# Optimization experiments

Measured on AMD Instinct MI355X. Metric: run time of the kernel, lower is better.

Reference implementation:

```python
import jax, jax.numpy as jnp
import numpy as np

IN_FEATURES = 4096
OUT_FEATURES = 4096
GROUPS = 1
QB = 2 ** (8 - 1) - 1  # 127, int8 absmax quant


def setup_inputs() -> dict:
    key = jax.random.key(0)
    k_x, k_w = jax.random.split(key)
    x = jax.random.normal(k_x, (8192, IN_FEATURES), dtype=jnp.float32)
    # kaiming_uniform_(a=sqrt(5)) -> uniform(-1/sqrt(in), 1/sqrt(in))
    bound = 1.0 / np.sqrt(IN_FEATURES)
    weight = jax.random.uniform(
        k_w, (OUT_FEATURES, IN_FEATURES), dtype=jnp.float32,
        minval=-bound, maxval=bound)
    return {"input": x, "weight": weight}


def reference(input, weight):
    # --- ternarize weight per group ---
    w = weight.reshape(GROUPS, -1)                       # [G, out*in/G]
    w = w - jnp.mean(w, axis=1, keepdims=True)
    w = jnp.sign(w)
    # beta: per-group scale (note denominator uses full element count, as in source)
    beta = jnp.sum(jnp.abs(w), axis=1, keepdims=True) / (w.shape[0] * w.shape[1])
    w = (w * beta).reshape(OUT_FEATURES, IN_FEATURES)    # [out, in]

    # --- absmax int8 quantize activations (quantized values used, not dequant) ---
    scale = QB / jnp.max(jnp.abs(input))
    quant = jnp.round(scale * input)                     # [tokens, in]

    # --- linear + rescale ---
    out = quant @ w.T                                    # [tokens, out]
    out = out / beta.reshape(-1, 1)                      # groups=1: scalar divide
    return out
```

## Files before the change

### kernel.cpp

```cpp
#include <hip/hip_runtime.h>
#include <hip/hip_bf16.h>

typedef __attribute__((ext_vector_type(4))) int int4v;

#define TOKENS 8192
#define IN_F   4096
#define OUT_F  4096


__global__ __launch_bounds__(256) void k_pre(const float4* __restrict__ w,
                                             const float4* __restrict__ x,
                                             double* __restrict__ partials,
                                             float* __restrict__ xpart) {
  if (blockIdx.x < 1024) {
    __shared__ double sm[256];
    double s = 0.0;
    const float4* p = w + (size_t)blockIdx.x * 4096;
    for (int i = threadIdx.x; i < 4096; i += 256) {
      float4 v = p[i];
      s += (double)v.x + (double)v.y + (double)v.z + (double)v.w;
    }
    sm[threadIdx.x] = s;
    __syncthreads();
    for (int off = 128; off > 0; off >>= 1) {
      if (threadIdx.x < off) sm[threadIdx.x] += sm[threadIdx.x + off];
      __syncthreads();
    }
    if (threadIdx.x == 0) partials[blockIdx.x] = sm[0];
  } else {
    const int b = blockIdx.x - 1024;
    float m = 0.f;
    const size_t n = (size_t)TOKENS * IN_F / 4;
    for (size_t i = (size_t)b * 256 + threadIdx.x; i < n; i += (size_t)1024 * 256) {
      float4 v = x[i];
      m = fmaxf(m, fmaxf(fmaxf(fabsf(v.x), fabsf(v.y)),
                         fmaxf(fabsf(v.z), fabsf(v.w))));
    }
    __shared__ float smf[256];
    smf[threadIdx.x] = m;
    __syncthreads();
    for (int off = 128; off > 0; off >>= 1) {
      if (threadIdx.x < off) smf[threadIdx.x] = fmaxf(smf[threadIdx.x], smf[threadIdx.x + off]);
      __syncthreads();
    }
    if (threadIdx.x == 0) xpart[b] = smf[0];
  }
}

__global__ __launch_bounds__(256) void k_finalize(double* __restrict__ hdr,
                                                  const double* __restrict__ partials,
                                                  const float* __restrict__ xpart) {
  __shared__ double sm[256];
  __shared__ float smf[256];
  double s = partials[threadIdx.x] + partials[threadIdx.x + 256] +
             partials[threadIdx.x + 512] + partials[threadIdx.x + 768];
  float m = fmaxf(fmaxf(xpart[threadIdx.x], xpart[threadIdx.x + 256]),
                  fmaxf(xpart[threadIdx.x + 512], xpart[threadIdx.x + 768]));
  sm[threadIdx.x] = s;
  smf[threadIdx.x] = m;
  __syncthreads();
  for (int off = 128; off > 0; off >>= 1) {
    if (threadIdx.x < off) {
      sm[threadIdx.x] += sm[threadIdx.x + off];
      smf[threadIdx.x] = fmaxf(smf[threadIdx.x], smf[threadIdx.x + off]);
    }
    __syncthreads();
  }
  if (threadIdx.x == 0) {
    hdr[0] = sm[0] / (double)((size_t)OUT_F * IN_F);
    hdr[1] = 127.0 / (double)smf[0];
  }
}

#define QB_BLK ((TOKENS * IN_F / 4) / 256)
#define TB_BLK ((OUT_F * IN_F / 4) / 256)
__global__ __launch_bounds__(256) void k_quant_tern(const float4* __restrict__ x,
                                                    const float4* __restrict__ w,
                                                    int* __restrict__ q,
                                                    int* __restrict__ sgn,
                                                    const double* __restrict__ hdr) {
  if (blockIdx.x < QB_BLK) {
    const double s = hdr[1];
    size_t i = (size_t)blockIdx.x * 256 + threadIdx.x;
    float4 v = x[i];
    int a = (int)rint(s * (double)v.x);
    int b = (int)rint(s * (double)v.y);
    int c = (int)rint(s * (double)v.z);
    int d = (int)rint(s * (double)v.w);
    q[i] = (a & 255) | ((b & 255) << 8) | ((c & 255) << 16) | ((d & 255) << 24);
  } else {
    const double m = hdr[0];
    size_t i = (size_t)(blockIdx.x - QB_BLK) * 256 + threadIdx.x;
    float4 v = w[i];
    int a = ((double)v.x > m) - ((double)v.x < m);
    int b = ((double)v.y > m) - ((double)v.y < m);
    int c = ((double)v.z > m) - ((double)v.z < m);
    int d = ((double)v.w > m) - ((double)v.w < m);
    sgn[i] = (a & 255) | ((b & 255) << 8) | ((c & 255) << 16) | ((d & 255) << 24);
  }
}

__global__ __launch_bounds__(512, 2) void k_gemm(const signed char* __restrict__ q,
                                                 const signed char* __restrict__ s,
                                                 float* __restrict__ out) {
  __shared__ signed char sA[4][256 * 64];
  __shared__ signed char sB[4][256 * 64];
  const int tid  = threadIdx.x;
  const int lane = tid & 63;
  const int wid  = tid >> 6;
  const int wm   = wid >> 2;
  const int wn   = wid & 3;
  const int l15  = lane & 15, l4 = lane >> 4;

  const int swz = (blockIdx.x & 7) * 64 + (blockIdx.x >> 3);
  const int bm = swz >> 4;
  const int bn = swz & 15;
  const size_t row0 = (size_t)bm * 256;
  const size_t col0 = (size_t)bn * 256;

  const int lane_off = l15 * 64 + ((l4 ^ ((l15 >> 1) & 3)) << 4);

#define SB0() __builtin_amdgcn_sched_barrier(0)

#define STAGE_AB(KT, BUF)                                                       \
  do {                                                                          \
    const int kt_ = (KT);                                                       \
    _Pragma("unroll")                                                           \
    for (int u = 0; u < 2; ++u) {                                               \
      const int slot = u * 512 + tid;                                           \
      const int r = slot >> 2, sir = slot & 3;                                  \
      const int koff = ((sir ^ ((r >> 1) & 3)) << 4);                           \
      const int ldst = (u * 512 + wid * 64) * 16;                               \
      __builtin_amdgcn_global_load_lds(                                         \
          (const __attribute__((address_space(1))) void*)(q + (row0 + (size_t)r) * IN_F + kt_ * 64 + koff), \
          (__attribute__((address_space(3))) void*)(sA[BUF] + ldst), 16, 0, 0); \
    }                                                                           \
    _Pragma("unroll")                                                           \
    for (int u = 0; u < 2; ++u) {                                               \
      const int slot = u * 512 + tid;                                           \
      const int r = slot >> 2, sir = slot & 3;                                  \
      const int koff = ((sir ^ ((r >> 1) & 3)) << 4);                           \
      const int ldst = (u * 512 + wid * 64) * 16;                               \
      __builtin_amdgcn_global_load_lds(                                         \
          (const __attribute__((address_space(1))) void*)(s + (col0 + (size_t)r) * IN_F + kt_ * 64 + koff), \
          (__attribute__((address_space(3))) void*)(sB[BUF] + ldst), 16, 0, 0); \
    }                                                                           \
  } while (0)

#define READ12(BUF, AV, BV)                                                     \
  do {                                                                          \
    _Pragma("unroll")                                                           \
    for (int f = 0; f < 8; ++f)                                                 \
      AV[f] = *(const int4v*)(sA[BUF] + (wm * 128 + f * 16) * 64 + lane_off);   \
    _Pragma("unroll")                                                           \
    for (int f = 0; f < 4; ++f)                                                 \
      BV[f] = *(const int4v*)(sB[BUF] + (wn * 64 + f * 16) * 64 + lane_off);    \
  } while (0)

#define MFMA32(AV, BV)                                                          \
  do {                                                                          \
    _Pragma("unroll")                                                           \
    for (int m_ = 0; m_ < 8; ++m_)                                              \
      _Pragma("unroll")                                                         \
      for (int n_ = 0; n_ < 4; ++n_)                                            \
        acc[m_][n_] = __builtin_amdgcn_mfma_i32_16x16x64_i8(AV[m_], BV[n_],     \
                                                            acc[m_][n_], 0, 0, 0); \
  } while (0)

#define BODY(KT, RBUF, SBUF, ACUR, BCUR, ANXT, BNXT)                            \
  do {                                                                          \
    asm volatile("s_waitcnt vmcnt(4)" ::: "memory");                            \
    SB0();                                                                      \
    __builtin_amdgcn_s_barrier();                                               \
    SB0();                                                                      \
    READ12(RBUF, ANXT, BNXT);                                                   \
    STAGE_AB(((KT) + 3) & 63, SBUF);                                            \
    SB0();                                                                      \
    asm volatile("s_waitcnt lgkmcnt(12)" ::: "memory");                         \
    SB0();                                                                      \
    __builtin_amdgcn_s_setprio(1);                                              \
    MFMA32(ACUR, BCUR);                                                         \
    __builtin_amdgcn_s_setprio(0);                                              \
    SB0();                                                                      \
  } while (0)

  int4v acc[8][4];
#pragma unroll
  for (int i = 0; i < 8; ++i)
#pragma unroll
    for (int j = 0; j < 4; ++j) acc[i][j] = int4v{0, 0, 0, 0};

  int4v aX[8], bX[4], aY[8], bY[4];

  STAGE_AB(0, 0);
  STAGE_AB(1, 1);
  STAGE_AB(2, 2);
  SB0();
  asm volatile("s_waitcnt vmcnt(8)" ::: "memory");
  SB0();
  __builtin_amdgcn_s_barrier();
  SB0();
  READ12(0, aX, bX);
  SB0();

  for (int kt = 0; kt < 64; kt += 4) {
    BODY(kt + 0, 1, 3, aX, bX, aY, bY);
    BODY(kt + 1, 2, 0, aY, bY, aX, bX);
    BODY(kt + 2, 3, 1, aX, bX, aY, bY);
    BODY(kt + 3, 0, 2, aY, bY, aX, bX);
  }

#pragma unroll
  for (int m = 0; m < 8; ++m)
#pragma unroll
    for (int n = 0; n < 4; ++n)
#pragma unroll
      for (int r = 0; r < 4; ++r) {
        const size_t rg = row0 + wm * 128 + m * 16 + l4 * 4 + r;
        const size_t cg = col0 + wn * 64 + n * 16 + l15;
        out[rg * OUT_F + cg] = (float)acc[m][n][r];
      }

#undef SB0
#undef STAGE_AB
#undef READ12
#undef MFMA32
#undef BODY
}

extern "C" void kernel_launch(void* const* d_in, const int* in_sizes, int n_in,
                              void* d_out, int out_size, void* d_ws, size_t ws_size,
                              hipStream_t stream) {
  const float* x = (const float*)d_in[0];
  const float* w = (const float*)d_in[1];
  float* out = (float*)d_out;

  char* ws = (char*)d_ws;
  double*   hdr      = (double*)ws;
  double*   partials = (double*)(ws + 1024);
  float*    xpart    = (float*)(ws + 9216);
  signed char* qbuf  = (signed char*)(ws + 16384);
  signed char* sbuf  = (signed char*)(ws + 16384 + (size_t)TOKENS * IN_F);

  k_pre<<<2048, 256, 0, stream>>>((const float4*)w, (const float4*)x, partials, xpart);
  k_finalize<<<1, 256, 0, stream>>>(hdr, partials, xpart);
  k_quant_tern<<<QB_BLK + TB_BLK, 256, 0, stream>>>((const float4*)x, (const float4*)w,
                                                    (int*)qbuf, (int*)sbuf, hdr);
  k_gemm<<<(TOKENS / 256) * (OUT_F / 256), 512, 0, stream>>>(qbuf, sbuf, out);
}
```

Baseline: 227.1 us.

## Restructure int8 GEMM mainloop to double-buffered K=128 tiles with ping-pong phases

Replaces the 4-stage K=64 LDS ring with a 2-stage ring of K=128 tiles and splits each tile's work into four barrier-separated MFMA phases. Global-to-LDS staging for A and B is interleaved between the phases. The LDS swizzle changes to an 8-way XOR over 128-byte rows. The aim is to halve the number of main-loop iterations and overlap loads with compute in a ping-pong style. In exchange it adds several extra barriers per tile, uses full vmcnt(0) waits, and keeps less prefetch depth in flight.

```diff
diff --git a/kernel.cpp b/kernel.cpp
--- a/kernel.cpp
+++ b/kernel.cpp
@@ -103,8 +103,8 @@
 __global__ __launch_bounds__(512, 2) void k_gemm(const signed char* __restrict__ q,
                                                  const signed char* __restrict__ s,
                                                  float* __restrict__ out) {
-  __shared__ signed char sA[4][256 * 64];
-  __shared__ signed char sB[4][256 * 64];
+  __shared__ signed char sA[2][256 * 128];
+  __shared__ signed char sB[2][256 * 128];
   const int tid  = threadIdx.x;
   const int lane = tid & 63;
   const int wid  = tid >> 6;
@@ -118,70 +118,99 @@
   const size_t row0 = (size_t)bm * 256;
   const size_t col0 = (size_t)bn * 256;
 
-  const int lane_off = l15 * 64 + ((l4 ^ ((l15 >> 1) & 3)) << 4);
+  const int xr = l15 & 7;
+  const int ksl0 = ((l4 ^ xr) << 4);
+  const int ksl1 = (((4 + l4) ^ xr) << 4);
+  const int aRowBase = (wm * 128 + l15) * 128;
+  const int bRowBase = (wn * 64 + l15) * 128;
 
 #define SB0() __builtin_amdgcn_sched_barrier(0)
 
-#define STAGE_AB(KT, BUF)                                                       \
+#define STAGE_T(GSRC, GROW0, KT, LDSBASE)                                       \
   do {                                                                          \
     const int kt_ = (KT);                                                       \
     _Pragma("unroll")                                                           \
-    for (int u = 0; u < 2; ++u) {                                               \
-      const int slot = u * 512 + tid;                                           \
-      const int r = slot >> 2, sir = slot & 3;                                  \
-      const int koff = ((sir ^ ((r >> 1) & 3)) << 4);                           \
-      const int ldst = (u * 512 + wid * 64) * 16;                               \
+    for (int u = 0; u < 4; ++u) {                                               \
+      const int d = u * 512 + tid;                                              \
+      const int r = d >> 3, p = d & 7;                                          \
+      const int koff = ((p ^ (r & 7)) << 4);                                    \
       __builtin_amdgcn_global_load_lds(                                         \
-          (const __attribute__((address_space(1))) void*)(q + (row0 + (size_t)r) * IN_F + kt_ * 64 + koff), \
-          (__attribute__((address_space(3))) void*)(sA[BUF] + ldst), 16, 0, 0); \
+          (const __attribute__((address_space(1))) void*)((GSRC) + ((GROW0) + (size_t)r) * IN_F + kt_ * 128 + koff), \
+          (__attribute__((address_space(3))) void*)((LDSBASE) + (u * 512 + wid * 64) * 16), 16, 0, 0); \
     }                                                                           \
-    _Pragma("unroll")                                                           \
-    for (int u = 0; u < 2; ++u) {                                               \
-      const int slot = u * 512 + tid;                                           \
-      const int r = slot >> 2, sir = slot & 3;                                  \
-      const int koff = ((sir ^ ((r >> 1) & 3)) << 4);                           \
-      const int ldst = (u * 512 + wid * 64) * 16;                               \
-      __builtin_amdgcn_global_load_lds(                                         \
-          (const __attribute__((address_space(1))) void*)(s + (col0 + (size_t)r) * IN_F + kt_ * 64 + koff), \
-          (__attribute__((address_space(3))) void*)(sB[BUF] + ldst), 16, 0, 0); \
-    }                                                                           \
-  } while (0)
-
-#define READ12(BUF, AV, BV)                                                     \
+  } while (0)
+
+#define RD_A8(BUF, AV, KSL)                                                     \
   do {                                                                          \
     _Pragma("unroll")                                                           \
     for (int f = 0; f < 8; ++f)                                                 \
-      AV[f] = *(const int4v*)(sA[BUF] + (wm * 128 + f * 16) * 64 + lane_off);   \
+      AV[f] = *(const int4v*)(sA[BUF] + aRowBase + f * 2048 + (KSL));           \
+  } while (0)
+
+#define RD_B2(BUF, BV, NB0, KSL)                                                \
+  do {                                                                          \
+    BV[0] = *(const int4v*)(sB[BUF] + bRowBase + (NB0) * 2048 + (KSL));         \
+    BV[1] = *(const int4v*)(sB[BUF] + bRowBase + ((NB0) + 1) * 2048 + (KSL));   \
+  } while (0)
+
+#define MFMA16(AV, BV, NB)                                                      \
+  do {                                                                          \
     _Pragma("unroll")                                                           \
-    for (int f = 0; f < 4; ++f)                                                 \
-      BV[f] = *(const int4v*)(sB[BUF] + (wn * 64 + f * 16) * 64 + lane_off);    \
-  } while (0)
-
-#define MFMA32(AV, BV)                                                          \
-  do {                                                                          \
-    _Pragma("unroll")                                                           \
-    for (int m_ = 0; m_ < 8; ++m_)                                              \
-      _Pragma("unroll")                                                         \
-      for (int n_ = 0; n_ < 4; ++n_)                                            \
-        acc[m_][n_] = __builtin_amdgcn_mfma_i32_16x16x64_i8(AV[m_], BV[n_],     \
-                                                            acc[m_][n_], 0, 0, 0); \
-  } while (0)
-
-#define BODY(KT, RBUF, SBUF, ACUR, BCUR, ANXT, BNXT)                            \
-  do {                                                                          \
-    asm volatile("s_waitcnt vmcnt(4)" ::: "memory");                            \
+    for (int m_ = 0; m_ < 8; ++m_) {                                            \
+      acc[m_][NB]     = __builtin_amdgcn_mfma_i32_16x16x64_i8(AV[m_], BV[0],    \
+                                                              acc[m_][NB], 0, 0, 0); \
+      acc[m_][NB + 1] = __builtin_amdgcn_mfma_i32_16x16x64_i8(AV[m_], BV[1],    \
+                                                              acc[m_][NB + 1], 0, 0, 0); \
+    }                                                                           \
+  } while (0)
+
+#define PH_ENTER()                                                              \
+  SB0();                                                                        \
+  __builtin_amdgcn_s_barrier();                                                 \
+  asm volatile("s_waitcnt lgkmcnt(0)" ::: "memory");                            \
+  SB0();                                                                        \
+  __builtin_amdgcn_s_setprio(1)
+
+#define PH_EXIT()                                                               \
+  __builtin_amdgcn_s_setprio(0);                                                \
+  SB0();                                                                        \
+  __builtin_amdgcn_s_barrier()
+
+#define BODY(KT, CUR, NXT)                                                      \
+  do {                                                                          \
+                          \
+    RD_A8(CUR, a0, ksl0);                                                       \
+    RD_B2(CUR, bb, 0, ksl0);                                                    \
+    STAGE_T(q, row0, ((KT) + 1) & 31, sA[NXT]);                                 \
+    PH_ENTER();                                                                 \
+    MFMA16(a0, bb, 0);                                                          \
+    PH_EXIT();                                                                  \
+                                     \
+    RD_B2(CUR, bb, 2, ksl0);                                                    \
+    STAGE_T(s, col0, ((KT) + 1) & 31, sB[NXT]);                                 \
+    PH_ENTER();                                                                 \
+    MFMA16(a0, bb, 2);                                                          \
+    PH_EXIT();                                                                  \
+                                         \
+    RD_A8(CUR, a1, ksl1);                                                       \
+    RD_B2(CUR, bb, 0, ksl1);                                                    \
+    PH_ENTER();                                                                 \
+    MFMA16(a1, bb, 0);                                                          \
+    PH_EXIT();                                                                  \
+         \
+    RD_B2(CUR, bb, 2, ksl1);                                                    \
     SB0();                                                                      \
     __builtin_amdgcn_s_barrier();                                               \
-    SB0();                                                                      \
-    READ12(RBUF, ANXT, BNXT);                                                   \
-    STAGE_AB(((KT) + 3) & 63, SBUF);                                            \
-    SB0();                                                                      \
-    asm volatile("s_waitcnt lgkmcnt(12)" ::: "memory");                         \
+    asm volatile("s_waitcnt lgkmcnt(0)" ::: "memory");                          \
     SB0();                                                                      \
     __builtin_amdgcn_s_setprio(1);                                              \
-    MFMA32(ACUR, BCUR);                                                         \
+    MFMA16(a1, bb, 2);                                                          \
     __builtin_amdgcn_s_setprio(0);                                              \
     SB0();                                                                      \
+    asm volatile("s_waitcnt vmcnt(0)" ::: "memory");                            \
+    SB0();                                                                      \
+    __builtin_amdgcn_s_barrier();                                               \
+    SB0();                                                                      \
   } while (0)
 
   int4v acc[8][4];
@@ -190,24 +219,19 @@
 #pragma unroll
     for (int j = 0; j < 4; ++j) acc[i][j] = int4v{0, 0, 0, 0};
 
-  int4v aX[8], bX[4], aY[8], bY[4];
-
-  STAGE_AB(0, 0);
-  STAGE_AB(1, 1);
-  STAGE_AB(2, 2);
+  int4v a0[8], a1[8], bb[2];
+
+  STAGE_T(q, row0, 0, sA[0]);
+  STAGE_T(s, col0, 0, sB[0]);
   SB0();
-  asm volatile("s_waitcnt vmcnt(8)" ::: "memory");
+  asm volatile("s_waitcnt vmcnt(0)" ::: "memory");
   SB0();
   __builtin_amdgcn_s_barrier();
   SB0();
-  READ12(0, aX, bX);
-  SB0();
-
-  for (int kt = 0; kt < 64; kt += 4) {
-    BODY(kt + 0, 1, 3, aX, bX, aY, bY);
-    BODY(kt + 1, 2, 0, aY, bY, aX, bX);
-    BODY(kt + 2, 3, 1, aX, bX, aY, bY);
-    BODY(kt + 3, 0, 2, aY, bY, aX, bX);
+
+  for (int kt = 0; kt < 32; kt += 2) {
+    BODY(kt + 0, 0, 1);
+    BODY(kt + 1, 1, 0);
   }
 
 #pragma unroll
@@ -222,9 +246,12 @@
       }
 
 #undef SB0
-#undef STAGE_AB
-#undef READ12
-#undef MFMA32
+#undef STAGE_T
+#undef RD_A8
+#undef RD_B2
+#undef MFMA16
+#undef PH_ENTER
+#undef PH_EXIT
 #undef BODY
 }
 
```

New measurement: 222.4 us. -2.0%, faster.
